# Kernel optimization log

Measured on AMD Instinct MI355X. Metric: run time of the kernel, lower is better.

## Reference

```python
import jax, jax.numpy as jnp
import numpy as np

EPS = 1e-6
NUM_HEADS = 16
ROPE_THETA = 100000.0


def _rope_tables(seq_len, head_dim, theta):
    inv_freq = 1.0 / (theta ** (np.arange(0, head_dim, 2, dtype=np.float32) / head_dim))
    t = np.arange(seq_len, dtype=np.float32)
    freqs = np.outer(t, inv_freq)                      # (S, head_dim//2)
    emb = np.concatenate([freqs, freqs], axis=-1)      # (S, head_dim)
    return jnp.asarray(np.cos(emb))[None], jnp.asarray(np.sin(emb))[None]  # (1,S,D)


def setup_inputs() -> dict:
    key = jax.random.key(0)
    ks = jax.random.split(key, 6)
    B, S, H = 2, 2048, 1024
    head_dim = H // NUM_HEADS
    cos, sin = _rope_tables(S, head_dim, ROPE_THETA)
    scale = 0.02
    return {
        "hidden_states": jax.random.normal(ks[0], (B, S, H), dtype=jnp.float32),
        "cos": cos, "sin": sin,
        "Wq": jax.random.normal(ks[1], (H, H), dtype=jnp.float32) * scale,
        "bq": jnp.zeros((H,), dtype=jnp.float32),
        "Wk": jax.random.normal(ks[2], (H, H), dtype=jnp.float32) * scale,
        "bk": jnp.zeros((H,), dtype=jnp.float32),
        "Wv": jax.random.normal(ks[3], (H, H), dtype=jnp.float32) * scale,
        "bv": jnp.zeros((H,), dtype=jnp.float32),
        "Wo": jax.random.normal(ks[4], (H, H), dtype=jnp.float32) * scale,
        "bo": jnp.zeros((H,), dtype=jnp.float32),
        "rms_weight": jnp.ones((H,), dtype=jnp.float32),
    }


def _rms_norm(x, w):
    var = jnp.mean(x * x, axis=-1, keepdims=True)
    return x * jax.lax.rsqrt(var + EPS) * w


def _rotate_half(x):
    x1, x2 = jnp.split(x, 2, axis=-1)
    return jnp.concatenate([-x2, x1], axis=-1)


def reference(hidden_states, cos, sin, Wq, bq, Wk, bk, Wv, bv, Wo, bo, rms_weight):
    B, S, H = hidden_states.shape
    D = H // NUM_HEADS
    q = hidden_states @ Wq.T + bq
    k = hidden_states @ Wk.T + bk
    v = hidden_states @ Wv.T + bv
    # RMSNorm over full hidden dim BEFORE head split (as in original)
    q = _rms_norm(q, rms_weight)
    k = _rms_norm(k, rms_weight)
    # (B,S,H) -> (B,heads,S,D)
    q = q.reshape(B, S, NUM_HEADS, D).transpose(0, 2, 1, 3)
    k = k.reshape(B, S, NUM_HEADS, D).transpose(0, 2, 1, 3)
    v = v.reshape(B, S, NUM_HEADS, D).transpose(0, 2, 1, 3)
    # RoPE: cos/sin (1,S,D) -> unsqueeze head dim
    c = cos[:, None, :, :]
    s = sin[:, None, :, :]
    q = q * c + _rotate_half(q) * s
    k = k * c + _rotate_half(k) * s
    # attention (faithful: boolean tril mask is ADDED as 0/1, not -inf)
    scale = D ** 0.5
    scores = jnp.einsum("bhqd,bhkd->bhqk", q, k) / scale
    mask = jnp.tril(jnp.ones((S, S), dtype=scores.dtype))  # +1 on causal, +0 elsewhere
    attn = jax.nn.softmax(scores + mask, axis=-1)
    out = jnp.einsum("bhqk,bhkd->bhqd", attn, v)
    out = out.transpose(0, 2, 1, 3).reshape(B, S, H)
    return out @ Wo.T + bo
```

## Files before the change

kernel.cpp:

```cpp
#include <hip/hip_runtime.h>

typedef unsigned short u16;
typedef __attribute__((ext_vector_type(8))) _Float16 half8;
typedef __attribute__((ext_vector_type(2))) __fp16 fp16x2;
typedef __attribute__((ext_vector_type(4))) float f32x4;
typedef __attribute__((ext_vector_type(16))) float f32x16;

#define MFMAH(A,B,C) __builtin_amdgcn_mfma_f32_16x16x32_f16(A,B,C,0,0,0)
#define MFMA32(A,B,C) __builtin_amdgcn_mfma_f32_32x32x16_f16(A,B,C,0,0,0)
#define LOG2E 1.4426950408889634f
#define C1 0.18033688011112042f

__device__ __forceinline__ u16 f2h(float f){
  _Float16 h = (_Float16)f; u16 r; __builtin_memcpy(&r,&h,2); return r;
}
__device__ __forceinline__ float h2f(u16 v){
  _Float16 h; __builtin_memcpy(&h,&v,2); return (float)h;
}
__device__ __forceinline__ unsigned int pack_h2(float a, float b){
  fp16x2 h = __builtin_amdgcn_cvt_pkrtz(a,b);
  unsigned int r; __builtin_memcpy(&r,&h,4); return r;
}

__device__ __forceinline__ void async_ld16(const void* g, void* l) {
  __builtin_amdgcn_global_load_lds(
      (const __attribute__((address_space(1))) unsigned int*)g,
      (__attribute__((address_space(3))) unsigned int*)l, 16, 0, 0);
}

__global__ __launch_bounds__(256) void cast_all(const float* __restrict__ hs,
    const float* __restrict__ wq, const float* __restrict__ wk,
    const float* __restrict__ wv, const float* __restrict__ wo,
    u16* __restrict__ dst)
{
  unsigned int i = blockIdx.x*256 + threadIdx.x;
  size_t el = (size_t)i * 8;
  const float* src; size_t off;
  if (el < 4194304) { src = hs; off = el; }
  else {
    unsigned int r = (unsigned int)((el - 4194304) >> 20);
    src = (r==0)?wq:(r==1)?wk:(r==2)?wv:wo;
    off = (el - 4194304) & 1048575;
  }
  float4 a = *reinterpret_cast<const float4*>(src+off);
  float4 b = *reinterpret_cast<const float4*>(src+off+4);
  uint4 o = {pack_h2(a.x,a.y), pack_h2(a.z,a.w), pack_h2(b.x,b.y), pack_h2(b.z,b.w)};
  *reinterpret_cast<uint4*>(dst + el) = o;
}

__global__ __launch_bounds__(256) void gemm_qkv(const u16* __restrict__ A,
                                                const u16* __restrict__ W,
                                                const float* __restrict__ bqp,
                                                const float* __restrict__ bkp,
                                                const float* __restrict__ bvp,
                                                u16* __restrict__ qout,
                                                u16* __restrict__ kout,
                                                u16* __restrict__ vout,
                                                int M, int K)
{
  __shared__ __align__(16) u16 lds_a[128*32];
  __shared__ __align__(16) u16 lds_w[128*32];
  const int t = threadIdx.x;
  const int lane = t & 63, wave = t >> 6;
  const int wm = wave >> 1, wn = wave & 1;
  const int lr = lane & 15, quad = lane >> 4;
  const int flat = blockIdx.x;
  const int xcd = flat & 7, slot = flat >> 3;
  const int ln = slot % 12, lm = slot / 12;
  const int n0 = ((xcd & 1) * 12 + ln) * 128;
  const int m0 = ((xcd >> 1) * 8 + lm) * 128;
  const int wbase = t & 192;
  const int which = n0 >> 10;

  const f32x4 fzero = {0.f,0.f,0.f,0.f};
  f32x4 acc[4][4];
  #pragma unroll
  for (int i=0;i<4;++i)
    #pragma unroll
    for (int j=0;j<4;++j) acc[i][j] = fzero;

  if (which < 2) {
    for (int k0 = 0; k0 < K; k0 += 32) {
      __syncthreads();
      #pragma unroll
      for (int it=0; it<2; ++it) {
        int idx = it*256 + t;
        int row = idx >> 2, c8 = (idx & 3) * 8;
        int lbase = (it*256 + wbase) * 8;
        async_ld16(&A[(size_t)(m0+row)*K + k0 + c8], &lds_a[lbase]);
        async_ld16(&W[(size_t)(n0+row)*K + k0 + c8], &lds_w[lbase]);
      }
      __syncthreads();
      half8 af[4], bfr[4];
      #pragma unroll
      for (int mt=0; mt<4; ++mt)
        af[mt] = *reinterpret_cast<const half8*>(&lds_a[(wm*64 + mt*16 + lr)*32 + quad*8]);
      #pragma unroll
      for (int nt=0; nt<4; ++nt)
        bfr[nt] = *reinterpret_cast<const half8*>(&lds_w[(wn*64 + nt*16 + lr)*32 + quad*8]);
      #pragma unroll
      for (int mt=0; mt<4; ++mt)
        #pragma unroll
        for (int nt=0; nt<4; ++nt)
          acc[mt][nt] = MFMAH(bfr[nt], af[mt], acc[mt][nt]);
    }
    const float* bp = which ? bkp : bqp;
    u16* dst = which ? kout : qout;
    #pragma unroll
    for (int nt=0; nt<4; ++nt) {
      int nn = (n0 & 1023) + wn*64 + nt*16 + quad*4;
      float4 bv = *reinterpret_cast<const float4*>(&bp[nn]);
      int hh = nn >> 6, d4 = nn & 63;
      #pragma unroll
      for (int mt=0; mt<4; ++mt) {
        int m = m0 + wm*64 + mt*16 + lr;
        int b = m >> 11, s = m & 2047;
        uint2 o = {pack_h2(acc[mt][nt][0]+bv.x, acc[mt][nt][1]+bv.y),
                   pack_h2(acc[mt][nt][2]+bv.z, acc[mt][nt][3]+bv.w)};
        *reinterpret_cast<uint2*>(&dst[((size_t)(b*16 + hh)*2048 + s)*64 + d4]) = o;
      }
    }
  } else {
    for (int k0 = 0; k0 < K; k0 += 32) {
      __syncthreads();
      #pragma unroll
      for (int it=0; it<2; ++it) {
        int idx = it*256 + t;
        int row = idx >> 2, c8 = (idx & 3) * 8;
        int lbase = (it*256 + wbase) * 8;
        async_ld16(&A[(size_t)(m0+row)*K + k0 + c8], &lds_a[lbase]);
        async_ld16(&W[(size_t)(n0+row)*K + k0 + c8], &lds_w[lbase]);
      }
      __syncthreads();
      half8 af[4], bfr[4];
      #pragma unroll
      for (int mt=0; mt<4; ++mt)
        af[mt] = *reinterpret_cast<const half8*>(&lds_a[(wm*64 + mt*16 + lr)*32 + quad*8]);
      #pragma unroll
      for (int nt=0; nt<4; ++nt)
        bfr[nt] = *reinterpret_cast<const half8*>(&lds_w[(wn*64 + nt*16 + lr)*32 + quad*8]);
      #pragma unroll
      for (int mt=0; mt<4; ++mt)
        #pragma unroll
        for (int nt=0; nt<4; ++nt)
          acc[mt][nt] = MFMAH(af[mt], bfr[nt], acc[mt][nt]);
    }
    #pragma unroll
    for (int nt=0; nt<4; ++nt) {
      int nn = (n0 & 1023) + wn*64 + nt*16 + lr;
      float bv = bvp[nn];
      int hh = nn >> 6, d = nn & 63;
      #pragma unroll
      for (int mt=0; mt<4; ++mt) {
        int m = m0 + wm*64 + mt*16 + quad*4;
        int b = m >> 11, s = m & 2047;
        uint2 o = {pack_h2(acc[mt][nt][0]+bv, acc[mt][nt][1]+bv),
                   pack_h2(acc[mt][nt][2]+bv, acc[mt][nt][3]+bv)};
        *reinterpret_cast<uint2*>(&vout[((size_t)(b*16 + hh)*64 + d)*2048 + s]) = o;
      }
    }
  }
}

__global__ __launch_bounds__(256) void gemm_o(const u16* __restrict__ A,
                                              const u16* __restrict__ W,
                                              const float* __restrict__ bias,
                                              float* __restrict__ O,
                                              int M, int N, int K)
{
  __shared__ __align__(16) u16 lds_a[128*32];
  __shared__ __align__(16) u16 lds_w[64*32];
  const int t = threadIdx.x;
  const int lane = t & 63, wm = t >> 6;
  const int lr = lane & 15, quad = lane >> 4;
  const int flat = blockIdx.x;
  const int xcd = flat & 7, slot = flat >> 3;
  const int n0 = (slot & 15) * 64;
  const int m0 = ((xcd << 2) + (slot >> 4)) * 128;
  const int wbase = t & 192;

  const f32x4 fzero = {0.f,0.f,0.f,0.f};
  f32x4 acc[2][4];
  #pragma unroll
  for (int i=0;i<2;++i)
    #pragma unroll
    for (int j=0;j<4;++j) acc[i][j] = fzero;

  for (int k0 = 0; k0 < K; k0 += 32) {
    __syncthreads();
    #pragma unroll
    for (int it=0; it<2; ++it) {
      int idx = it*256 + t;
      int row = idx >> 2, c8 = (idx & 3) * 8;
      int lbase = (it*256 + wbase) * 8;
      async_ld16(&A[(size_t)(m0+row)*K + k0 + c8], &lds_a[lbase]);
    }
    async_ld16(&W[(size_t)(n0 + (t>>2))*K + k0 + (t&3)*8], &lds_w[wbase*8]);
    __syncthreads();
    half8 af[2], bfr[4];
    #pragma unroll
    for (int mt=0; mt<2; ++mt)
      af[mt] = *reinterpret_cast<const half8*>(&lds_a[(wm*32 + mt*16 + lr)*32 + quad*8]);
    #pragma unroll
    for (int nt=0; nt<4; ++nt)
      bfr[nt] = *reinterpret_cast<const half8*>(&lds_w[(nt*16 + lr)*32 + quad*8]);
    #pragma unroll
    for (int mt=0; mt<2; ++mt)
      #pragma unroll
      for (int nt=0; nt<4; ++nt)
        acc[mt][nt] = MFMAH(bfr[nt], af[mt], acc[mt][nt]);
  }

  #pragma unroll
  for (int nt=0; nt<4; ++nt) {
    int nb = n0 + nt*16 + quad*4;
    float4 bv = *reinterpret_cast<const float4*>(&bias[nb]);
    #pragma unroll
    for (int mt=0; mt<2; ++mt) {
      int m = m0 + wm*32 + mt*16 + lr;
      float4 o = {acc[mt][nt][0]+bv.x, acc[mt][nt][1]+bv.y,
                  acc[mt][nt][2]+bv.z, acc[mt][nt][3]+bv.w};
      *reinterpret_cast<float4*>(&O[(size_t)m * N + nb]) = o;
    }
  }
}

__global__ __launch_bounds__(256) void rmsrope(u16* __restrict__ qb, u16* __restrict__ kb,
                                               const float* __restrict__ cosb,
                                               const float* __restrict__ sinb,
                                               const float* __restrict__ w)
{
  const int bs = blockIdx.x;
  const int b = bs >> 11, s = bs & 2047;
  const int t = threadIdx.x;
  u16* buf = (t & 128) ? kb : qb;
  const int tl = t & 127;
  const int h = tl >> 3, d0 = (tl & 7) * 4;
  size_t base = ((size_t)(b*16+h)*2048 + s)*64;

  uint2 u1 = *reinterpret_cast<const uint2*>(&buf[base + d0]);
  uint2 u2 = *reinterpret_cast<const uint2*>(&buf[base + d0 + 32]);
  u16 a1[4], a2[4];
  __builtin_memcpy(a1, &u1, 8); __builtin_memcpy(a2, &u2, 8);
  float x1[4], x2[4];
  float ss = 0.f;
  #pragma unroll
  for (int j=0;j<4;++j){
    x1[j] = h2f(a1[j]); x2[j] = h2f(a2[j]);
    ss += x1[j]*x1[j] + x2[j]*x2[j];
  }
  #pragma unroll
  for (int off=32; off>0; off>>=1) ss += __shfl_xor(ss, off, 64);
  __shared__ float red[4];
  if ((t & 63) == 0) red[t>>6] = ss;
  __syncthreads();
  float tot = (t & 128) ? (red[2] + red[3]) : (red[0] + red[1]);
  float r = rsqrtf(tot * (1.0f/1024.0f) + 1e-6f);

  float4 w1 = *reinterpret_cast<const float4*>(&w[h*64+d0]);
  float4 w2 = *reinterpret_cast<const float4*>(&w[h*64+d0+32]);
  float4 c1 = *reinterpret_cast<const float4*>(&cosb[s*64+d0]);
  float4 s1 = *reinterpret_cast<const float4*>(&sinb[s*64+d0]);
  float4 c2 = *reinterpret_cast<const float4*>(&cosb[s*64+d0+32]);
  float4 s2 = *reinterpret_cast<const float4*>(&sinb[s*64+d0+32]);
  float n1[4] = {x1[0]*r*w1.x, x1[1]*r*w1.y, x1[2]*r*w1.z, x1[3]*r*w1.w};
  float n2[4] = {x2[0]*r*w2.x, x2[1]*r*w2.y, x2[2]*r*w2.z, x2[3]*r*w2.w};
  float o1[4] = {n1[0]*c1.x - n2[0]*s1.x, n1[1]*c1.y - n2[1]*s1.y,
                 n1[2]*c1.z - n2[2]*s1.z, n1[3]*c1.w - n2[3]*s1.w};
  float o2[4] = {n2[0]*c2.x + n1[0]*s2.x, n2[1]*c2.y + n1[1]*s2.y,
                 n2[2]*c2.z + n1[2]*s2.z, n2[3]*c2.w + n1[3]*s2.w};
  uint2 v1 = {pack_h2(o1[0],o1[1]), pack_h2(o1[2],o1[3])};
  uint2 v2 = {pack_h2(o2[0],o2[1]), pack_h2(o2[2],o2[3])};
  *reinterpret_cast<uint2*>(&buf[base + d0])      = v1;
  *reinterpret_cast<uint2*>(&buf[base + d0 + 32]) = v2;
}

__global__ __launch_bounds__(512, 1) void attn(const u16* __restrict__ qh,
                                               const u16* __restrict__ kh,
                                               const u16* __restrict__ vt,
                                               u16* __restrict__ ao)
{
  __shared__ __align__(16) u16 kbuf[2][2][64*72];
  __shared__ __align__(16) u16 vbuf[2][2][64*72];
  const int t = threadIdx.x;
  const int lane = t & 63, w = t >> 6;
  const int g = w >> 2, wq = w & 3;
  const int ql = lane & 31, hf = lane >> 5;
  const int flat = blockIdx.x;
  const int xcd = flat & 7, slot = flat >> 3;
  const int bh = xcd + ((slot >> 3) << 3);
  const int qbase = (slot & 7) * 256;
  const int b = bh >> 4, h = bh & 15;
  const size_t hb = (size_t)bh * 2048 * 64;
  const u16* qp = qh + hb;
  const u16* kp = kh + hb;
  const u16* vtp = vt + hb;

  half8 qf[2][4];
  #pragma unroll
  for (int qh2=0; qh2<2; ++qh2) {
    int qa = qbase + wq*64 + qh2*32 + ql;
    #pragma unroll
    for (int s=0;s<4;++s)
      qf[qh2][s] = *reinterpret_cast<const half8*>(&qp[(size_t)qa*64 + s*16 + hf*8]);
  }

  const int lt = t & 255;
  const int row = lt >> 3;
  const int cc = lt & 7;
  const int base2 = 32*(cc>>2) + 16*((cc>>1)&1) + 4*(cc&1);
  const int kofs = row*72 + cc*8;
  const u16* kg = kp + (size_t)(g*1024 + row)*64 + cc*8;
  const u16* vg = vtp + (size_t)row*2048 + g*1024 + base2;

  const f32x16 fz16 = {0.f,0.f,0.f,0.f,0.f,0.f,0.f,0.f,0.f,0.f,0.f,0.f,0.f,0.f,0.f,0.f};
  f32x16 oacc[2][2];
  oacc[0][0]=fz16; oacc[0][1]=fz16; oacc[1][0]=fz16; oacc[1][1]=fz16;
  float lsum[2] = {0.f, 0.f};
  const int diag = (qbase + wq*64) >> 6;

  {
    uint4 k0v = *reinterpret_cast<const uint4*>(kg);
    uint4 k1v = *reinterpret_cast<const uint4*>(kg + 32*64);
    uint2 a0 = *reinterpret_cast<const uint2*>(vg);
    uint2 a1 = *reinterpret_cast<const uint2*>(vg + 8);
    uint2 b0 = *reinterpret_cast<const uint2*>(vg + (size_t)32*2048);
    uint2 b1 = *reinterpret_cast<const uint2*>(vg + (size_t)32*2048 + 8);
    *reinterpret_cast<uint4*>(&kbuf[g][0][kofs])        = k0v;
    *reinterpret_cast<uint4*>(&kbuf[g][0][kofs+32*72])  = k1v;
    uint4 v0 = {a0.x,a0.y,a1.x,a1.y};
    uint4 v1 = {b0.x,b0.y,b1.x,b1.y};
    *reinterpret_cast<uint4*>(&vbuf[g][0][kofs])        = v0;
    *reinterpret_cast<uint4*>(&vbuf[g][0][kofs+32*72])  = v1;
  }

  for (int kt=0; kt<16; ++kt) {
    __syncthreads();
    uint4 k0n, k1n; uint2 a0n, a1n, b0n, b1n;
    if (kt < 15) {
      const u16* kgn = kg + (size_t)(kt+1)*4096;
      const u16* vgn = vg + (kt+1)*64;
      k0n = *reinterpret_cast<const uint4*>(kgn);
      k1n = *reinterpret_cast<const uint4*>(kgn + 32*64);
      a0n = *reinterpret_cast<const uint2*>(vgn);
      a1n = *reinterpret_cast<const uint2*>(vgn + 8);
      b0n = *reinterpret_cast<const uint2*>(vgn + (size_t)32*2048);
      b1n = *reinterpret_cast<const uint2*>(vgn + (size_t)32*2048 + 8);
    }
    const u16* kb = &kbuf[g][kt & 1][0];
    const u16* vb = &vbuf[g][kt & 1][0];
    const int gkt = (g << 4) + kt;

    unsigned int pk[2][4][4];
    #pragma unroll
    for (int kh2=0; kh2<2; ++kh2) {
      half8 kf[4];
      #pragma unroll
      for (int s=0;s<4;++s)
        __builtin_memcpy(&kf[s], &kb[(kh2*32+ql)*72 + s*16 + hf*8], 16);
      f32x16 z0 = fz16, z1 = fz16;
      #pragma unroll
      for (int s=0;s<4;++s) z0 = MFMA32(kf[s], qf[0][s], z0);
      #pragma unroll
      for (int s=0;s<4;++s) z1 = MFMA32(kf[s], qf[1][s], z1);

      #pragma unroll
      for (int qh2=0; qh2<2; ++qh2) {
        const f32x16& z = qh2 ? z1 : z0;
        const int qa = qbase + wq*64 + qh2*32 + ql;
        float p[16];
        if (gkt != diag) {
          float ml = (gkt < diag) ? LOG2E : 0.0f;
          #pragma unroll
          for (int r=0;r<16;++r)
            p[r] = __builtin_amdgcn_exp2f(__builtin_fmaf(z[r], C1, ml));
        } else {
          #pragma unroll
          for (int r=0;r<16;++r) {
            int key = gkt*64 + kh2*32 + (r&3) + 8*(r>>2) + 4*hf;
            float ml = (key <= qa) ? LOG2E : 0.0f;
            p[r] = __builtin_amdgcn_exp2f(__builtin_fmaf(z[r], C1, ml));
          }
        }
        float ls0=0.f, ls1=0.f, ls2=0.f, ls3=0.f;
        #pragma unroll
        for (int r=0;r<16;r+=4){ ls0+=p[r]; ls1+=p[r+1]; ls2+=p[r+2]; ls3+=p[r+3]; }
        lsum[qh2] += (ls0+ls1)+(ls2+ls3);
        #pragma unroll
        for (int t2=0;t2<2;++t2)
          #pragma unroll
          for (int jj=0;jj<4;++jj)
            pk[qh2][kh2*2+t2][jj] = pack_h2(p[t2*8+jj*2], p[t2*8+jj*2+1]);
      }
    }

    #pragma unroll
    for (int st=0;st<4;++st) {
      half8 vf0, vf1;
      __builtin_memcpy(&vf0, &vb[(0*32+ql)*72 + st*16 + hf*8], 16);
      __builtin_memcpy(&vf1, &vb[(1*32+ql)*72 + st*16 + hf*8], 16);
      #pragma unroll
      for (int qh2=0; qh2<2; ++qh2) {
        uint4 pq = {pk[qh2][st][0], pk[qh2][st][1], pk[qh2][st][2], pk[qh2][st][3]};
        half8 pf; __builtin_memcpy(&pf, &pq, 16);
        oacc[qh2][0] = MFMA32(vf0, pf, oacc[qh2][0]);
        oacc[qh2][1] = MFMA32(vf1, pf, oacc[qh2][1]);
      }
    }

    if (kt < 15) {
      u16* kwn = &kbuf[g][(kt+1)&1][kofs];
      u16* vwn = &vbuf[g][(kt+1)&1][kofs];
      *reinterpret_cast<uint4*>(kwn)         = k0n;
      *reinterpret_cast<uint4*>(kwn + 32*72) = k1n;
      uint4 v0 = {a0n.x,a0n.y,a1n.x,a1n.y};
      uint4 v1 = {b0n.x,b0n.y,b1n.x,b1n.y};
      *reinterpret_cast<uint4*>(vwn)         = v0;
      *reinterpret_cast<uint4*>(vwn + 32*72) = v1;
    }
  }

  lsum[0] += __shfl_xor(lsum[0], 32, 64);
  lsum[1] += __shfl_xor(lsum[1], 32, 64);

  __syncthreads();
  f32x4* xch0 = (f32x4*)&kbuf[0][0][0];
  f32x4* xch1 = (f32x4*)&vbuf[0][0][0];
  float* xls  = (float*)((char*)&vbuf[0][0][0] + 32768);
  const int idx = wq*64 + lane;
  if (g == 1) {
    #pragma unroll
    for (int qh2=0; qh2<2; ++qh2) {
      f32x4* xch = qh2 ? xch1 : xch0;
      #pragma unroll
      for (int dh=0; dh<2; ++dh)
        #pragma unroll
        for (int rq=0; rq<4; ++rq) {
          f32x4 v = {oacc[qh2][dh][rq*4+0], oacc[qh2][dh][rq*4+1],
                     oacc[qh2][dh][rq*4+2], oacc[qh2][dh][rq*4+3]};
          xch[(dh*4+rq)*256 + idx] = v;
        }
      xls[qh2*256 + idx] = lsum[qh2];
    }
  }
  __syncthreads();
  if (g == 0) {
    #pragma unroll
    for (int qh2=0; qh2<2; ++qh2) {
      f32x4* xch = qh2 ? xch1 : xch0;
      float inv = 1.0f / (lsum[qh2] + xls[qh2*256 + idx]);
      int qa = qbase + wq*64 + qh2*32 + ql;
      size_t rowbase = ((size_t)(b*2048 + qa))*1024 + h*64;
      #pragma unroll
      for (int dh=0; dh<2; ++dh)
        #pragma unroll
        for (int rq=0; rq<4; ++rq) {
          int dd = dh*32 + 8*rq + 4*hf;
          f32x4 v = xch[(dh*4+rq)*256 + idx];
          uint2 o = {pack_h2((oacc[qh2][dh][rq*4+0]+v.x)*inv, (oacc[qh2][dh][rq*4+1]+v.y)*inv),
                     pack_h2((oacc[qh2][dh][rq*4+2]+v.z)*inv, (oacc[qh2][dh][rq*4+3]+v.w)*inv)};
          *reinterpret_cast<uint2*>(&ao[rowbase + dd]) = o;
        }
    }
  }
}

extern "C" void kernel_launch(void* const* d_in, const int* in_sizes, int n_in,
                              void* d_out, int out_size, void* d_ws, size_t ws_size,
                              hipStream_t stream)
{
  const float* hs   = (const float*)d_in[0];
  const float* cosb = (const float*)d_in[1];
  const float* sinb = (const float*)d_in[2];
  const float* Wq   = (const float*)d_in[3];
  const float* bq   = (const float*)d_in[4];
  const float* Wk   = (const float*)d_in[5];
  const float* bk   = (const float*)d_in[6];
  const float* Wv   = (const float*)d_in[7];
  const float* bv   = (const float*)d_in[8];
  const float* Wo   = (const float*)d_in[9];
  const float* bo   = (const float*)d_in[10];
  const float* rw   = (const float*)d_in[11];

  const size_t NEL = (size_t)4096 * 1024;
  const size_t WEL = (size_t)1024 * 1024;
  u16* hsb = (u16*)d_ws;
  u16* wqb = hsb + NEL;
  u16* wob = wqb + 3*WEL;
  u16* qhb = wob + WEL;
  u16* khb = qhb + NEL;
  u16* vtb = khb + NEL;
  u16* aob = hsb;

  cast_all<<<4096, 256, 0, stream>>>(hs, Wq, Wk, Wv, Wo, hsb);
  gemm_qkv<<<768, 256, 0, stream>>>(hsb, wqb, bq, bk, bv, qhb, khb, vtb, 4096, 1024);
  rmsrope<<<4096, 256, 0, stream>>>(qhb, khb, cosb, sinb, rw);
  attn<<<256, 512, 0, stream>>>(qhb, khb, vtb, aob);
  gemm_o<<<512, 256, 0, stream>>>(aob, wob, bo, (float*)d_out, 4096, 1024, 1024);
}
```

Before: 213.3 us.

## Software-pipeline PV MFMAs of previous tile with QK of current tile

Restructures the attention inner loop so the P·V matrix multiplies for the previous key tile are interleaved between the two halves of the current tile's Q·K multiplies. The probabilities for the previous tile are kept in registers, and a final P·V step runs after the loop. The V shared-memory buffer grows from double to triple buffering so the tile still being read is never overwritten by the prefetch. The aim is to overlap MFMA work with the exp/softmax VALU work and LDS latency, at the cost of more live registers and more shared memory.

```diff
diff --git a/kernel.cpp b/kernel.cpp
--- a/kernel.cpp
+++ b/kernel.cpp
@@ -281,7 +281,7 @@
                                                u16* __restrict__ ao)
 {
   __shared__ __align__(16) u16 kbuf[2][2][64*72];
-  __shared__ __align__(16) u16 vbuf[2][2][64*72];
+  __shared__ __align__(16) u16 vbuf[2][3][64*72];
   const int t = threadIdx.x;
   const int lane = t & 63, w = t >> 6;
   const int g = w >> 2, wq = w & 3;
@@ -317,6 +317,7 @@
   f32x16 oacc[2][2];
   oacc[0][0]=fz16; oacc[0][1]=fz16; oacc[1][0]=fz16; oacc[1][1]=fz16;
   float lsum[2] = {0.f, 0.f};
+  unsigned int pkp[2][4][4];
   const int diag = (qbase + wq*64) >> 6;
 
   {
@@ -334,6 +335,9 @@
     *reinterpret_cast<uint4*>(&vbuf[g][0][kofs+32*72])  = v1;
   }
 
+  int vs_r = 2;
+  int vs_w = 1;
+
   for (int kt=0; kt<16; ++kt) {
     __syncthreads();
     uint4 k0n, k1n; uint2 a0n, a1n, b0n, b1n;
@@ -348,25 +352,66 @@
       b1n = *reinterpret_cast<const uint2*>(vgn + (size_t)32*2048 + 8);
     }
     const u16* kb = &kbuf[g][kt & 1][0];
-    const u16* vb = &vbuf[g][kt & 1][0];
+    const u16* vbr = &vbuf[g][vs_r][0];
     const int gkt = (g << 4) + kt;
 
-    unsigned int pk[2][4][4];
+    half8 kf0[4];
+    #pragma unroll
+    for (int s=0;s<4;++s)
+      __builtin_memcpy(&kf0[s], &kb[(0*32+ql)*72 + s*16 + hf*8], 16);
+    f32x16 z00 = fz16, z01 = fz16;
+    #pragma unroll
+    for (int s=0;s<4;++s) z00 = MFMA32(kf0[s], qf[0][s], z00);
+    #pragma unroll
+    for (int s=0;s<4;++s) z01 = MFMA32(kf0[s], qf[1][s], z01);
+
+    if (kt > 0) {
+      #pragma unroll
+      for (int st=0; st<2; ++st) {
+        half8 vf0, vf1;
+        __builtin_memcpy(&vf0, &vbr[(0*32+ql)*72 + st*16 + hf*8], 16);
+        __builtin_memcpy(&vf1, &vbr[(1*32+ql)*72 + st*16 + hf*8], 16);
+        #pragma unroll
+        for (int qh2=0; qh2<2; ++qh2) {
+          uint4 pq = {pkp[qh2][st][0], pkp[qh2][st][1], pkp[qh2][st][2], pkp[qh2][st][3]};
+          half8 pf; __builtin_memcpy(&pf, &pq, 16);
+          oacc[qh2][0] = MFMA32(vf0, pf, oacc[qh2][0]);
+          oacc[qh2][1] = MFMA32(vf1, pf, oacc[qh2][1]);
+        }
+      }
+    }
+
+    half8 kf1[4];
+    #pragma unroll
+    for (int s=0;s<4;++s)
+      __builtin_memcpy(&kf1[s], &kb[(1*32+ql)*72 + s*16 + hf*8], 16);
+    f32x16 z10 = fz16, z11 = fz16;
+    #pragma unroll
+    for (int s=0;s<4;++s) z10 = MFMA32(kf1[s], qf[0][s], z10);
+    #pragma unroll
+    for (int s=0;s<4;++s) z11 = MFMA32(kf1[s], qf[1][s], z11);
+
+    if (kt > 0) {
+      #pragma unroll
+      for (int st=2; st<4; ++st) {
+        half8 vf0, vf1;
+        __builtin_memcpy(&vf0, &vbr[(0*32+ql)*72 + st*16 + hf*8], 16);
+        __builtin_memcpy(&vf1, &vbr[(1*32+ql)*72 + st*16 + hf*8], 16);
+        #pragma unroll
+        for (int qh2=0; qh2<2; ++qh2) {
+          uint4 pq = {pkp[qh2][st][0], pkp[qh2][st][1], pkp[qh2][st][2], pkp[qh2][st][3]};
+          half8 pf; __builtin_memcpy(&pf, &pq, 16);
+          oacc[qh2][0] = MFMA32(vf0, pf, oacc[qh2][0]);
+          oacc[qh2][1] = MFMA32(vf1, pf, oacc[qh2][1]);
+        }
+      }
+    }
+
     #pragma unroll
     for (int kh2=0; kh2<2; ++kh2) {
-      half8 kf[4];
-      #pragma unroll
-      for (int s=0;s<4;++s)
-        __builtin_memcpy(&kf[s], &kb[(kh2*32+ql)*72 + s*16 + hf*8], 16);
-      f32x16 z0 = fz16, z1 = fz16;
-      #pragma unroll
-      for (int s=0;s<4;++s) z0 = MFMA32(kf[s], qf[0][s], z0);
-      #pragma unroll
-      for (int s=0;s<4;++s) z1 = MFMA32(kf[s], qf[1][s], z1);
-
       #pragma unroll
       for (int qh2=0; qh2<2; ++qh2) {
-        const f32x16& z = qh2 ? z1 : z0;
+        const f32x16& z = kh2 ? (qh2 ? z11 : z10) : (qh2 ? z01 : z00);
         const int qa = qbase + wq*64 + qh2*32 + ql;
         float p[16];
         if (gkt != diag) {
@@ -390,33 +435,39 @@
         for (int t2=0;t2<2;++t2)
           #pragma unroll
           for (int jj=0;jj<4;++jj)
-            pk[qh2][kh2*2+t2][jj] = pack_h2(p[t2*8+jj*2], p[t2*8+jj*2+1]);
-      }
-    }
-
-    #pragma unroll
-    for (int st=0;st<4;++st) {
-      half8 vf0, vf1;
-      __builtin_memcpy(&vf0, &vb[(0*32+ql)*72 + st*16 + hf*8], 16);
-      __builtin_memcpy(&vf1, &vb[(1*32+ql)*72 + st*16 + hf*8], 16);
-      #pragma unroll
-      for (int qh2=0; qh2<2; ++qh2) {
-        uint4 pq = {pk[qh2][st][0], pk[qh2][st][1], pk[qh2][st][2], pk[qh2][st][3]};
-        half8 pf; __builtin_memcpy(&pf, &pq, 16);
-        oacc[qh2][0] = MFMA32(vf0, pf, oacc[qh2][0]);
-        oacc[qh2][1] = MFMA32(vf1, pf, oacc[qh2][1]);
+            pkp[qh2][kh2*2+t2][jj] = pack_h2(p[t2*8+jj*2], p[t2*8+jj*2+1]);
       }
     }
 
     if (kt < 15) {
       u16* kwn = &kbuf[g][(kt+1)&1][kofs];
-      u16* vwn = &vbuf[g][(kt+1)&1][kofs];
+      u16* vwn = &vbuf[g][vs_w][kofs];
       *reinterpret_cast<uint4*>(kwn)         = k0n;
       *reinterpret_cast<uint4*>(kwn + 32*72) = k1n;
       uint4 v0 = {a0n.x,a0n.y,a1n.x,a1n.y};
       uint4 v1 = {b0n.x,b0n.y,b1n.x,b1n.y};
       *reinterpret_cast<uint4*>(vwn)         = v0;
       *reinterpret_cast<uint4*>(vwn + 32*72) = v1;
+    }
+
+    vs_r = (vs_r == 2) ? 0 : vs_r + 1;
+    vs_w = (vs_w == 2) ? 0 : vs_w + 1;
+  }
+
+  {
+    const u16* vbr = &vbuf[g][0][0];
+    #pragma unroll
+    for (int st=0; st<4; ++st) {
+      half8 vf0, vf1;
+      __builtin_memcpy(&vf0, &vbr[(0*32+ql)*72 + st*16 + hf*8], 16);
+      __builtin_memcpy(&vf1, &vbr[(1*32+ql)*72 + st*16 + hf*8], 16);
+      #pragma unroll
+      for (int qh2=0; qh2<2; ++qh2) {
+        uint4 pq = {pkp[qh2][st][0], pkp[qh2][st][1], pkp[qh2][st][2], pkp[qh2][st][3]};
+        half8 pf; __builtin_memcpy(&pf, &pq, 16);
+        oacc[qh2][0] = MFMA32(vf0, pf, oacc[qh2][0]);
+        oacc[qh2][1] = MFMA32(vf1, pf, oacc[qh2][1]);
+      }
     }
   }
 
```

Result: no change. 215.3 us (+0.9%).
